# Performance work log

Measured on AMD Instinct MI355X. Metric: run time of the kernel, lower is better.

## Reference

```python
import jax, jax.numpy as jnp
import numpy as np

N_NODES = 50000
N_EDGES = 800000
N_GRAPHS = 128
IN_DIM, H1, H2, OUT_DIM = 256, 128, 64, 10


def setup_inputs() -> dict:
    key = jax.random.key(0)
    ks = jax.random.split(key, 8)
    x = jax.random.normal(ks[0], (N_NODES, IN_DIM), dtype=jnp.float32)
    edge_index = jax.random.randint(ks[1], (2, N_EDGES), 0, N_NODES, dtype=jnp.int64 if jax.config.jax_enable_x64 else jnp.int32)
    batch = jnp.sort(jax.random.randint(ks[2], (N_NODES,), 0, N_GRAPHS))
    s1 = 1.0 / np.sqrt(IN_DIM)
    s2 = 1.0 / np.sqrt(H1)
    s3 = 1.0 / np.sqrt(H2)
    W1 = jax.random.uniform(ks[3], (IN_DIM, H1), jnp.float32, -s1, s1)
    b1 = jnp.zeros((H1,), jnp.float32)
    W2 = jax.random.uniform(ks[4], (H1, H2), jnp.float32, -s2, s2)
    b2 = jnp.zeros((H2,), jnp.float32)
    Wfc = jax.random.uniform(ks[5], (H2, OUT_DIM), jnp.float32, -s3, s3)
    bfc = jax.random.uniform(ks[6], (OUT_DIM,), jnp.float32, -s3, s3)
    return {"x": x, "edge_index": edge_index, "batch": batch,
            "W1": W1, "b1": b1, "W2": W2, "b2": b2, "Wfc": Wfc, "bfc": bfc}


def _gcn_norm(edge_index, n_nodes):
    # PyG gcn_norm with add_self_loops=True: D^{-1/2} (A+I) D^{-1/2}
    self_loops = jnp.arange(n_nodes, dtype=edge_index.dtype)
    row = jnp.concatenate([edge_index[0], self_loops])
    col = jnp.concatenate([edge_index[1], self_loops])
    deg = jax.ops.segment_sum(jnp.ones_like(col, dtype=jnp.float32), col,
                              num_segments=n_nodes)
    dis = jnp.where(deg > 0, 1.0 / jnp.sqrt(deg), 0.0)
    norm = dis[row] * dis[col]  # [E + N]
    return row, col, norm


def _gcn_layer(x, W, b, row, col, norm, n_nodes):
    h = x @ W                          # [N, out]
    msg = h[row] * norm[:, None]       # gather + scale: [E+N, out]
    agg = jax.ops.segment_sum(msg, col, num_segments=n_nodes)
    return jax.nn.relu(agg + b)


def reference(x, edge_index, batch, W1, b1, W2, b2, Wfc, bfc):
    n = x.shape[0]
    row, col, norm = _gcn_norm(edge_index, n)
    h = _gcn_layer(x, W1, b1, row, col, norm, n)
    h = _gcn_layer(h, W2, b2, row, col, norm, n)
    # global max pool over graphs
    g = jax.ops.segment_max(h, batch, num_segments=N_GRAPHS)  # [G, H2]
    # dropout is identity at inference
    return g @ Wfc + bfc
```

## Files before the change

kernel.cpp:

```cpp
#include <hip/hip_runtime.h>
#include <math.h>


__global__ __launch_bounds__(256) void k_zero(int* __restrict__ cnt, int* __restrict__ pool,
                                              int n1, int n2) {
    int i = blockIdx.x * 256 + threadIdx.x;
    if (i < n1) cnt[i] = 0;
    if (i < n2) pool[i] = 0;
}

__global__ __launch_bounds__(256) void k_count(const int* __restrict__ ei, int* __restrict__ cnt,
                                               int E) {
    int e = blockIdx.x * 256 + threadIdx.x;
    if (e < E) atomicAdd(&cnt[ei[E + e]], 1);
}

__global__ __launch_bounds__(256) void k_dis(const int* __restrict__ cnt, float* __restrict__ dis,
                                             int N) {
    int v = blockIdx.x * 256 + threadIdx.x;
    if (v < N) dis[v] = 1.0f / sqrtf((float)(cnt[v] + 1));
}

__global__ __launch_bounds__(1024) void k_scan_block(const int* __restrict__ cnt,
                                                     int* __restrict__ rowptr,
                                                     int* __restrict__ bsum, int N) {
    __shared__ int lds[1024];
    int t = threadIdx.x;
    int i = blockIdx.x * 1024 + t;
    int val = (i < N) ? cnt[i] : 0;
    lds[t] = val;
    __syncthreads();
    for (int off = 1; off < 1024; off <<= 1) {
        int u = (t >= off) ? lds[t - off] : 0;
        __syncthreads();
        lds[t] += u;
        __syncthreads();
    }
    if (i < N) rowptr[i] = lds[t] - val;
    if (t == 1023) bsum[blockIdx.x] = lds[1023];
}

__global__ __launch_bounds__(1024) void k_scan_tot(const int* __restrict__ bsum,
                                                   int* __restrict__ bsum2, int nb) {
    __shared__ int lds[1024];
    int t = threadIdx.x;
    int val = (t < nb) ? bsum[t] : 0;
    lds[t] = val;
    __syncthreads();
    for (int off = 1; off < 1024; off <<= 1) {
        int u = (t >= off) ? lds[t - off] : 0;
        __syncthreads();
        lds[t] += u;
        __syncthreads();
    }
    if (t < nb) bsum2[t] = lds[t] - val;
}

__global__ __launch_bounds__(256) void k_scan_add(int* __restrict__ rowptr, int* __restrict__ cursor,
                                                  const int* __restrict__ bsum2, int N, int E) {
    int i = blockIdx.x * 256 + threadIdx.x;
    if (i < N) {
        int r = rowptr[i] + bsum2[i >> 10];
        rowptr[i] = r;
        cursor[i] = r;
    }
    if (i == 0) rowptr[N] = E;
}

__global__ __launch_bounds__(256) void k_fill(const int* __restrict__ ei,
                                              const float* __restrict__ dis,
                                              int* __restrict__ cursor,
                                              float2* __restrict__ csr, int E) {
    int e = blockIdx.x * 256 + threadIdx.x;
    if (e >= E) return;
    int r = ei[e];
    int c = ei[E + e];
    int p = atomicAdd(&cursor[c], 1);
    csr[p] = make_float2(__int_as_float(r), dis[r] * dis[c]);
}

template <int KDIM, int NOUT>
__global__ __launch_bounds__(256) void k_gemm(const float* __restrict__ A,
                                              const float* __restrict__ W,
                                              float* __restrict__ C, int M) {
    constexpr int BM = 64, BK = 32;
    constexpr int NGRP = NOUT / 64;
    __shared__ float As[BK][BM + 4];
    __shared__ float Ws[BK][NOUT];

    const int t = threadIdx.x;
    const int tx = t & 15;
    const int ty = t >> 4;
    const int row0 = blockIdx.x * BM;

    float acc[4][4 * NGRP];
#pragma unroll
    for (int r = 0; r < 4; r++)
#pragma unroll
        for (int c = 0; c < 4 * NGRP; c++) acc[r][c] = 0.f;

    for (int kc = 0; kc < KDIM; kc += BK) {
#pragma unroll
        for (int i = 0; i < 2; i++) {
            int s = t * 2 + i;
            int m = s >> 3;
            int kq = s & 7;
            int r = row0 + m;
            float4 v = make_float4(0.f, 0.f, 0.f, 0.f);
            if (r < M) v = *(const float4*)&A[(size_t)r * KDIM + kc + kq * 4];
            As[kq * 4 + 0][m] = v.x;
            As[kq * 4 + 1][m] = v.y;
            As[kq * 4 + 2][m] = v.z;
            As[kq * 4 + 3][m] = v.w;
        }
        constexpr int WLOADS = (BK * NOUT / 4) / 256;
#pragma unroll
        for (int i = 0; i < WLOADS; i++) {
            int s = t + i * 256;
            int k = s / (NOUT / 4);
            int c4 = s % (NOUT / 4);
            *(float4*)&Ws[k][c4 * 4] = *(const float4*)&W[(size_t)(kc + k) * NOUT + c4 * 4];
        }
        __syncthreads();

#pragma unroll
        for (int k = 0; k < BK; k++) {
            float4 a = *(const float4*)&As[k][ty * 4];
            float4 w0 = *(const float4*)&Ws[k][tx * 4];
            float4 w1;
            if (NGRP == 2) w1 = *(const float4*)&Ws[k][64 + tx * 4];
            const float* ap = (const float*)&a;
            const float* w0p = (const float*)&w0;
            const float* w1p = (const float*)&w1;
#pragma unroll
            for (int r = 0; r < 4; r++) {
#pragma unroll
                for (int c = 0; c < 4; c++) {
                    acc[r][c] += ap[r] * w0p[c];
                    if (NGRP == 2) acc[r][4 + c] += ap[r] * w1p[c];
                }
            }
        }
        __syncthreads();
    }

#pragma unroll
    for (int r = 0; r < 4; r++) {
        int rr = row0 + ty * 4 + r;
        if (rr < M) {
            float4 o0 = make_float4(acc[r][0], acc[r][1], acc[r][2], acc[r][3]);
            *(float4*)&C[(size_t)rr * NOUT + tx * 4] = o0;
            if (NGRP == 2) {
                float4 o1 = make_float4(acc[r][4], acc[r][5], acc[r][6], acc[r][7]);
                *(float4*)&C[(size_t)rr * NOUT + 64 + tx * 4] = o1;
            }
        }
    }
}

__global__ __launch_bounds__(256) void k_agg1(const float* __restrict__ h,
                                              const int* __restrict__ rowptr,
                                              const float2* __restrict__ csr,
                                              const float* __restrict__ dis,
                                              const float* __restrict__ b,
                                              float* __restrict__ out, int N) {
    int wave = (blockIdx.x * 256 + threadIdx.x) >> 6;
    int lane = threadIdx.x & 63;
    if (wave >= N) return;
    const int v = wave;
    const float2* hp = (const float2*)h;
    float d = dis[v];
    float ds2 = d * d;
    float2 hv = hp[(size_t)v * 64 + lane];
    float ax = ds2 * hv.x, ay = ds2 * hv.y;
    int s0 = rowptr[v], s1 = rowptr[v + 1];
    for (int j = s0; j < s1; j += 8) {
        int   uu[8];
        float ww[8];
#pragma unroll
        for (int q = 0; q < 8; q++) {
            int jj = j + q;
            bool ok = jj < s1;
            float2 e = csr[ok ? jj : s0];
            uu[q] = __float_as_int(e.x);
            ww[q] = ok ? e.y : 0.f;
        }
        float2 g[8];
#pragma unroll
        for (int q = 0; q < 8; q++) g[q] = hp[(size_t)uu[q] * 64 + lane];
#pragma unroll
        for (int q = 0; q < 8; q++) {
            ax += ww[q] * g[q].x;
            ay += ww[q] * g[q].y;
        }
    }
    float2 bb = *(const float2*)&b[lane * 2];
    float2 o;
    o.x = fmaxf(ax + bb.x, 0.f);
    o.y = fmaxf(ay + bb.y, 0.f);
    *(float2*)&out[(size_t)v * 128 + lane * 2] = o;
}

__global__ __launch_bounds__(256) void k_agg2_pool(const float* __restrict__ h,
                                                   const int* __restrict__ rowptr,
                                                   const float2* __restrict__ csr,
                                                   const float* __restrict__ dis,
                                                   const float* __restrict__ b,
                                                   const int* __restrict__ batch,
                                                   float* __restrict__ pool, int N) {
    int wave = (blockIdx.x * 256 + threadIdx.x) >> 6;
    int lane = threadIdx.x & 63;
    if (wave >= N) return;
    const int v = wave;
    float d = dis[v];
    float ds2 = d * d;
    float acc = ds2 * h[(size_t)v * 64 + lane];
    int s0 = rowptr[v], s1 = rowptr[v + 1];
    for (int j = s0; j < s1; j += 8) {
        int   uu[8];
        float ww[8];
#pragma unroll
        for (int q = 0; q < 8; q++) {
            int jj = j + q;
            bool ok = jj < s1;
            float2 e = csr[ok ? jj : s0];
            uu[q] = __float_as_int(e.x);
            ww[q] = ok ? e.y : 0.f;
        }
        float g[8];
#pragma unroll
        for (int q = 0; q < 8; q++) g[q] = h[(size_t)uu[q] * 64 + lane];
#pragma unroll
        for (int q = 0; q < 8; q++) acc += ww[q] * g[q];
    }
    float val = fmaxf(acc + b[lane], 0.f);
    int g = batch[v];
    atomicMax((int*)&pool[(size_t)g * 64 + lane], __float_as_int(val));
}

__global__ __launch_bounds__(256) void k_fc(const float* __restrict__ pool,
                                            const float* __restrict__ Wfc,
                                            const float* __restrict__ bfc,
                                            float* __restrict__ out, int G) {
    int t = blockIdx.x * 256 + threadIdx.x;
    if (t >= G * 10) return;
    int g = t / 10, o = t % 10;
    float acc = bfc[o];
#pragma unroll
    for (int f = 0; f < 64; f++) acc += pool[g * 64 + f] * Wfc[f * 10 + o];
    out[t] = acc;
}

extern "C" void kernel_launch(void* const* d_in, const int* in_sizes, int n_in,
                              void* d_out, int out_size, void* d_ws, size_t ws_size,
                              hipStream_t stream) {
    const float* x   = (const float*)d_in[0];
    const int*   ei  = (const int*)d_in[1];
    const int*   bat = (const int*)d_in[2];
    const float* W1  = (const float*)d_in[3];
    const float* b1  = (const float*)d_in[4];
    const float* W2  = (const float*)d_in[5];
    const float* b2  = (const float*)d_in[6];
    const float* Wfc = (const float*)d_in[7];
    const float* bfc = (const float*)d_in[8];
    float* out = (float*)d_out;

    const int N = in_sizes[2];
    const int E = in_sizes[1] / 2;
    const int G = out_size / 10;

    char* ws = (char*)d_ws;
    size_t off = 0;
    auto alloc = [&](size_t bytes) -> char* {
        char* p = ws + off;
        off = (off + bytes + 255) & ~(size_t)255;
        return p;
    };
    int*    cnt    = (int*)alloc((size_t)N * 4);
    float*  dis    = (float*)alloc((size_t)N * 4);
    int*    rowptr = (int*)alloc((size_t)(N + 1) * 4);
    int*    cursor = (int*)alloc((size_t)N * 4);
    int*    bsum   = (int*)alloc(1024 * 4);
    int*    bsum2  = (int*)alloc(1024 * 4);
    float2* csr    = (float2*)alloc((size_t)E * 8);
    float*  h      = (float*)alloc((size_t)N * 128 * 4);
    float*  a1     = (float*)alloc((size_t)N * 128 * 4);
    float*  pool   = (float*)alloc((size_t)G * 64 * 4);
    (void)ws_size; (void)n_in;

    const int nb = (N + 1023) / 1024;

    {
        int zmax = N > G * 64 ? N : G * 64;
        k_zero<<<(zmax + 255) / 256, 256, 0, stream>>>(cnt, (int*)pool, N, G * 64);
    }
    k_count<<<(E + 255) / 256, 256, 0, stream>>>(ei, cnt, E);
    k_dis<<<(N + 255) / 256, 256, 0, stream>>>(cnt, dis, N);
    k_scan_block<<<nb, 1024, 0, stream>>>(cnt, rowptr, bsum, N);
    k_scan_tot<<<1, 1024, 0, stream>>>(bsum, bsum2, nb);
    k_scan_add<<<(N + 255) / 256, 256, 0, stream>>>(rowptr, cursor, bsum2, N, E);
    k_fill<<<(E + 255) / 256, 256, 0, stream>>>(ei, dis, cursor, csr, E);

    k_gemm<256, 128><<<(N + 63) / 64, 256, 0, stream>>>(x, W1, h, N);
    k_agg1<<<(N * 64 + 255) / 256, 256, 0, stream>>>(h, rowptr, csr, dis, b1, a1, N);

    k_gemm<128, 64><<<(N + 63) / 64, 256, 0, stream>>>(a1, W2, h, N);
    k_agg2_pool<<<(N * 64 + 255) / 256, 256, 0, stream>>>(h, rowptr, csr, dis, b2, bat, pool, N);

    k_fc<<<(G * 10 + 255) / 256, 256, 0, stream>>>(pool, Wfc, bfc, out, G);
}
```

Measured before the change: 373.5 us.

## Use split-bf16 MFMA for first GEMM and prefetch CSR in aggregation

Replaces the fp32 SIMT GEMM for layer 1 with an MFMA kernel that splits each fp32 value into bf16 hi/lo parts and runs three bf16 MFMAs, keeping close to fp32 accuracy while using the matrix cores. A small kernel pre-splits and transposes W1 each call. The aggregation kernels now gather 16 neighbours per step and prefetch the next CSR chunk while the current gathers are in flight, to hide latency. This costs more registers and an extra launch, and the three-term split gives slightly lower precision than true fp32.

```diff
diff --git a/kernel.cpp b/kernel.cpp
--- a/kernel.cpp
+++ b/kernel.cpp
@@ -1,6 +1,21 @@
 #include <hip/hip_runtime.h>
 #include <math.h>
 
+
+typedef __attribute__((ext_vector_type(8))) short bfrag;
+typedef __attribute__((ext_vector_type(4))) float ffrag;
+
+__device__ inline void bf16split(float f, short& hi, short& lo) {
+    unsigned u = __float_as_uint(f);
+    unsigned r = u + 0x7fffu + ((u >> 16) & 1u);
+    unsigned short h = (unsigned short)(r >> 16);
+    float hf = __uint_as_float(((unsigned)h) << 16);
+    float lf = f - hf;
+    unsigned ul = __float_as_uint(lf);
+    unsigned rl = ul + 0x7fffu + ((ul >> 16) & 1u);
+    hi = (short)h;
+    lo = (short)(rl >> 16);
+}
 
 __global__ __launch_bounds__(256) void k_zero(int* __restrict__ cnt, int* __restrict__ pool,
                                               int n1, int n2) {
@@ -79,6 +94,97 @@
     csr[p] = make_float2(__int_as_float(r), dis[r] * dis[c]);
 }
 
+__global__ __launch_bounds__(256) void k_wsplit(const float* __restrict__ W,
+                                                short* __restrict__ wt_hi,
+                                                short* __restrict__ wt_lo) {
+    int i = blockIdx.x * 256 + threadIdx.x;
+    if (i >= 256 * 128) return;
+    int k = i >> 7, c = i & 127;
+    short hi, lo;
+    bf16split(W[i], hi, lo);
+    wt_hi[c * 256 + k] = hi;
+    wt_lo[c * 256 + k] = lo;
+}
+
+__global__ __launch_bounds__(256) void k_gemm1_mfma(const float* __restrict__ A,
+                                                    const short* __restrict__ wt_hi,
+                                                    const short* __restrict__ wt_lo,
+                                                    float* __restrict__ C, int M) {
+    constexpr int KD = 256;
+    __shared__ short Ah[64][40];
+    __shared__ short Al[64][40];
+
+    const int t = threadIdx.x;
+    const int lane = t & 63;
+    const int wid = t >> 6;
+    const int wr = wid >> 1;
+    const int wc = wid & 1;
+    const int row0 = blockIdx.x * 64;
+    const int lrow = lane & 15;
+    const int lkg = lane >> 4;
+
+    ffrag acc[2][4];
+#pragma unroll
+    for (int mr = 0; mr < 2; mr++)
+#pragma unroll
+        for (int nr = 0; nr < 4; nr++)
+#pragma unroll
+            for (int q = 0; q < 4; q++) acc[mr][nr][q] = 0.f;
+
+    for (int kc = 0; kc < KD; kc += 32) {
+#pragma unroll
+        for (int i = 0; i < 2; i++) {
+            int s = t * 2 + i;
+            int m = s >> 3;
+            int kq = s & 7;
+            int r = row0 + m;
+            float4 v = make_float4(0.f, 0.f, 0.f, 0.f);
+            if (r < M) v = *(const float4*)&A[(size_t)r * KD + kc + kq * 4];
+            short4 sh, sl;
+            bf16split(v.x, sh.x, sl.x);
+            bf16split(v.y, sh.y, sl.y);
+            bf16split(v.z, sh.z, sl.z);
+            bf16split(v.w, sh.w, sl.w);
+            *(short4*)&Ah[m][kq * 4] = sh;
+            *(short4*)&Al[m][kq * 4] = sl;
+        }
+        __syncthreads();
+
+        bfrag ahi[2], alo[2];
+#pragma unroll
+        for (int mr = 0; mr < 2; mr++) {
+            int arow = wr * 32 + mr * 16 + lrow;
+            ahi[mr] = *(const bfrag*)&Ah[arow][lkg * 8];
+            alo[mr] = *(const bfrag*)&Al[arow][lkg * 8];
+        }
+#pragma unroll
+        for (int nr = 0; nr < 4; nr++) {
+            int col = wc * 64 + nr * 16 + lrow;
+            const size_t boff = (size_t)col * 256 + kc + lkg * 8;
+            bfrag bhi = *(const bfrag*)&wt_hi[boff];
+            bfrag blo = *(const bfrag*)&wt_lo[boff];
+#pragma unroll
+            for (int mr = 0; mr < 2; mr++) {
+                acc[mr][nr] = __builtin_amdgcn_mfma_f32_16x16x32_bf16(ahi[mr], bhi, acc[mr][nr], 0, 0, 0);
+                acc[mr][nr] = __builtin_amdgcn_mfma_f32_16x16x32_bf16(ahi[mr], blo, acc[mr][nr], 0, 0, 0);
+                acc[mr][nr] = __builtin_amdgcn_mfma_f32_16x16x32_bf16(alo[mr], bhi, acc[mr][nr], 0, 0, 0);
+            }
+        }
+        __syncthreads();
+    }
+
+#pragma unroll
+    for (int mr = 0; mr < 2; mr++)
+#pragma unroll
+        for (int nr = 0; nr < 4; nr++)
+#pragma unroll
+            for (int q = 0; q < 4; q++) {
+                int rr = row0 + wr * 32 + mr * 16 + lkg * 4 + q;
+                int cc = wc * 64 + nr * 16 + lrow;
+                if (rr < M) C[(size_t)rr * 128 + cc] = acc[mr][nr][q];
+            }
+}
+
 template <int KDIM, int NOUT>
 __global__ __launch_bounds__(256) void k_gemm(const float* __restrict__ A,
                                               const float* __restrict__ W,
@@ -164,6 +270,7 @@
                                               const float* __restrict__ dis,
                                               const float* __restrict__ b,
                                               float* __restrict__ out, int N) {
+    constexpr int U = 16;
     int wave = (blockIdx.x * 256 + threadIdx.x) >> 6;
     int lane = threadIdx.x & 63;
     if (wave >= N) return;
@@ -174,24 +281,45 @@
     float2 hv = hp[(size_t)v * 64 + lane];
     float ax = ds2 * hv.x, ay = ds2 * hv.y;
     int s0 = rowptr[v], s1 = rowptr[v + 1];
-    for (int j = s0; j < s1; j += 8) {
-        int   uu[8];
-        float ww[8];
-#pragma unroll
-        for (int q = 0; q < 8; q++) {
-            int jj = j + q;
+
+    if (s0 < s1) {
+        int   uu[U];
+        float ww[U];
+#pragma unroll
+        for (int q = 0; q < U; q++) {
+            int jj = s0 + q;
             bool ok = jj < s1;
             float2 e = csr[ok ? jj : s0];
-            uu[q] = __float_as_int(e.x);
+            uu[q] = ok ? __float_as_int(e.x) : 0;
             ww[q] = ok ? e.y : 0.f;
         }
-        float2 g[8];
-#pragma unroll
-        for (int q = 0; q < 8; q++) g[q] = hp[(size_t)uu[q] * 64 + lane];
-#pragma unroll
-        for (int q = 0; q < 8; q++) {
-            ax += ww[q] * g[q].x;
-            ay += ww[q] * g[q].y;
+        for (int j = s0; j < s1; j += U) {
+            float2 g[U];
+#pragma unroll
+            for (int q = 0; q < U; q++) g[q] = hp[(size_t)uu[q] * 64 + lane];
+            int   uu2[U];
+            float ww2[U];
+            int jn = j + U;
+            if (jn < s1) {
+#pragma unroll
+                for (int q = 0; q < U; q++) {
+                    int jj = jn + q;
+                    bool ok = jj < s1;
+                    float2 e = csr[ok ? jj : s0];
+                    uu2[q] = ok ? __float_as_int(e.x) : 0;
+                    ww2[q] = ok ? e.y : 0.f;
+                }
+            } else {
+#pragma unroll
+                for (int q = 0; q < U; q++) { uu2[q] = 0; ww2[q] = 0.f; }
+            }
+#pragma unroll
+            for (int q = 0; q < U; q++) {
+                ax += ww[q] * g[q].x;
+                ay += ww[q] * g[q].y;
+            }
+#pragma unroll
+            for (int q = 0; q < U; q++) { uu[q] = uu2[q]; ww[q] = ww2[q]; }
         }
     }
     float2 bb = *(const float2*)&b[lane * 2];
@@ -208,6 +336,7 @@
                                                    const float* __restrict__ b,
                                                    const int* __restrict__ batch,
                                                    float* __restrict__ pool, int N) {
+    constexpr int U = 16;
     int wave = (blockIdx.x * 256 + threadIdx.x) >> 6;
     int lane = threadIdx.x & 63;
     if (wave >= N) return;
@@ -216,22 +345,43 @@
     float ds2 = d * d;
     float acc = ds2 * h[(size_t)v * 64 + lane];
     int s0 = rowptr[v], s1 = rowptr[v + 1];
-    for (int j = s0; j < s1; j += 8) {
-        int   uu[8];
-        float ww[8];
-#pragma unroll
-        for (int q = 0; q < 8; q++) {
-            int jj = j + q;
+
+    if (s0 < s1) {
+        int   uu[U];
+        float ww[U];
+#pragma unroll
+        for (int q = 0; q < U; q++) {
+            int jj = s0 + q;
             bool ok = jj < s1;
             float2 e = csr[ok ? jj : s0];
-            uu[q] = __float_as_int(e.x);
+            uu[q] = ok ? __float_as_int(e.x) : 0;
             ww[q] = ok ? e.y : 0.f;
         }
-        float g[8];
-#pragma unroll
-        for (int q = 0; q < 8; q++) g[q] = h[(size_t)uu[q] * 64 + lane];
-#pragma unroll
-        for (int q = 0; q < 8; q++) acc += ww[q] * g[q];
+        for (int j = s0; j < s1; j += U) {
+            float g[U];
+#pragma unroll
+            for (int q = 0; q < U; q++) g[q] = h[(size_t)uu[q] * 64 + lane];
+            int   uu2[U];
+            float ww2[U];
+            int jn = j + U;
+            if (jn < s1) {
+#pragma unroll
+                for (int q = 0; q < U; q++) {
+                    int jj = jn + q;
+                    bool ok = jj < s1;
+                    float2 e = csr[ok ? jj : s0];
+                    uu2[q] = ok ? __float_as_int(e.x) : 0;
+                    ww2[q] = ok ? e.y : 0.f;
+                }
+            } else {
+#pragma unroll
+                for (int q = 0; q < U; q++) { uu2[q] = 0; ww2[q] = 0.f; }
+            }
+#pragma unroll
+            for (int q = 0; q < U; q++) acc += ww[q] * g[q];
+#pragma unroll
+            for (int q = 0; q < U; q++) { uu[q] = uu2[q]; ww[q] = ww2[q]; }
+        }
     }
     float val = fmaxf(acc + b[lane], 0.f);
     int g = batch[v];
@@ -286,6 +436,8 @@
     float*  h      = (float*)alloc((size_t)N * 128 * 4);
     float*  a1     = (float*)alloc((size_t)N * 128 * 4);
     float*  pool   = (float*)alloc((size_t)G * 64 * 4);
+    short*  wt_hi  = (short*)alloc(128 * 256 * 2);
+    short*  wt_lo  = (short*)alloc(128 * 256 * 2);
     (void)ws_size; (void)n_in;
 
     const int nb = (N + 1023) / 1024;
@@ -294,6 +446,7 @@
         int zmax = N > G * 64 ? N : G * 64;
         k_zero<<<(zmax + 255) / 256, 256, 0, stream>>>(cnt, (int*)pool, N, G * 64);
     }
+    k_wsplit<<<128, 256, 0, stream>>>(W1, wt_hi, wt_lo);
     k_count<<<(E + 255) / 256, 256, 0, stream>>>(ei, cnt, E);
     k_dis<<<(N + 255) / 256, 256, 0, stream>>>(cnt, dis, N);
     k_scan_block<<<nb, 1024, 0, stream>>>(cnt, rowptr, bsum, N);
@@ -301,7 +454,7 @@
     k_scan_add<<<(N + 255) / 256, 256, 0, stream>>>(rowptr, cursor, bsum2, N, E);
     k_fill<<<(E + 255) / 256, 256, 0, stream>>>(ei, dis, cursor, csr, E);
 
-    k_gemm<256, 128><<<(N + 63) / 64, 256, 0, stream>>>(x, W1, h, N);
+    k_gemm1_mfma<<<(N + 63) / 64, 256, 0, stream>>>(x, wt_hi, wt_lo, h, N);
     k_agg1<<<(N * 64 + 255) / 256, 256, 0, stream>>>(h, rowptr, csr, dis, b1, a1, N);
 
     k_gemm<128, 64><<<(N + 63) / 64, 256, 0, stream>>>(a1, W2, h, N);
```

Result: slower. 412.5 us (+10.5%).
